# Kernel tuning notes

Hardware: AMD Instinct MI355X
Metric: run time of the kernel (lower is better)

Reference implementation:

```python
import math
import jax, jax.numpy as jnp
import numpy as np
from jax import lax

B, L, C_IN = 8, 1024, 64
D_MODEL, N_HEADS, D_FF, E_LAYERS, FACTOR = 512, 8, 2048, 3, 5


def conv1d_circ(x, w):
    # x [B,L,Cin], w [Cout,Cin,K]; torch Conv1d with padding_mode='circular'
    pad = (w.shape[-1] - 1) // 2
    xp = jnp.pad(x, ((0, 0), (pad, pad), (0, 0)), mode='wrap')
    return lax.conv_general_dilated(xp, jnp.transpose(w, (2, 1, 0)), (1,), 'VALID',
                                    dimension_numbers=('NWC', 'WIO', 'NWC'))


def pos_emb(Lq, d):
    pos = jnp.arange(Lq, dtype=jnp.float32)[:, None]
    div = jnp.exp(jnp.arange(0, d, 2, dtype=jnp.float32) * (-math.log(10000.0) / d))
    pe = jnp.zeros((Lq, d), dtype=jnp.float32)
    pe = pe.at[:, 0::2].set(jnp.sin(pos * div)).at[:, 1::2].set(jnp.cos(pos * div))
    return pe


def layer_norm(x, g, b, eps=1e-5):
    m = x.mean(-1, keepdims=True)
    v = ((x - m) ** 2).mean(-1, keepdims=True)
    return (x - m) / jnp.sqrt(v + eps) * g + b


def prob_attention(Q, K, V, rkey):
    # ProbSparse self-attention (mask_flag=False). Q,K,V: [B,H,L,D]
    Bq, H, Lq, D = Q.shape
    U = min(FACTOR * int(math.ceil(math.log(Lq))), Lq)  # sample_k == n_top since L_Q == L_K
    idx = jax.random.randint(rkey, (Lq, U), 0, Lq)       # per-query sampled key indices
    Ks = jnp.take(K, idx, axis=2)                        # [B,H,L,U,D]
    QKs = jnp.einsum('bhld,bhlud->bhlu', Q, Ks)          # sampled scores
    M = QKs.max(-1) - QKs.sum(-1) / Lq                   # sparsity measure (sum / L_K)
    _, top = lax.top_k(M, U)                             # [B,H,U] top-u query indices
    Qr = jnp.take_along_axis(Q, top[..., None], axis=2)  # [B,H,U,D]
    scores = jnp.einsum('bhud,bhld->bhul', Qr, K) * (1.0 / math.sqrt(D))
    attn = jax.nn.softmax(scores, axis=-1)
    upd = jnp.einsum('bhul,bhld->bhud', attn, V)
    # initial context = mean of V broadcast over queries; scatter updates at top-u
    ctx = jnp.broadcast_to(V.mean(axis=2, keepdims=True), (Bq, H, Lq, D))
    bi = jnp.arange(Bq)[:, None, None]
    hi = jnp.arange(H)[None, :, None]
    ctx = ctx.at[bi, hi, top].set(upd)
    return ctx


def attn_block(x, Wq, bq, Wk, bk, Wv, bv, Wo, bo, rkey):
    Bq, Lq, Dm = x.shape
    Dh = Dm // N_HEADS
    q = (x @ Wq.T + bq).reshape(Bq, Lq, N_HEADS, Dh).transpose(0, 2, 1, 3)
    k = (x @ Wk.T + bk).reshape(Bq, Lq, N_HEADS, Dh).transpose(0, 2, 1, 3)
    v = (x @ Wv.T + bv).reshape(Bq, Lq, N_HEADS, Dh).transpose(0, 2, 1, 3)
    ctx = prob_attention(q, k, v, rkey)
    out = ctx.transpose(0, 2, 1, 3).reshape(Bq, Lq, Dm)
    return out @ Wo.T + bo


def distil_conv(x, w, b, g, be):
    # Conv1d(k=3, circular) -> BatchNorm1d (batch stats) -> ELU -> MaxPool1d(3,2,1)
    y = conv1d_circ(x, w) + b
    mu = y.mean((0, 1))
    var = ((y - mu) ** 2).mean((0, 1))
    y = (y - mu) / jnp.sqrt(var + 1e-5) * g + be
    y = jax.nn.elu(y)
    y = lax.reduce_window(y, -jnp.inf, lax.max, (1, 3, 1), (1, 2, 1),
                          ((0, 0), (1, 1), (0, 0)))
    return y


def forward(x_enc, tok_w, Wq, bq, Wk, bk, Wv, bv, Wo, bo, c1w, c1b, c2w, c2b,
            n1g, n1b, n2g, n2b, dcw, dcb, bng, bnb, fng, fnb):
    x = x_enc + 1e-10
    x = conv1d_circ(x, tok_w) + pos_emb(x.shape[1], D_MODEL)  # embedding (dropout=0)
    for l in range(E_LAYERS):
        rkey = jax.random.fold_in(jax.random.key(42), l)
        x = x + attn_block(x, Wq[l], bq[l], Wk[l], bk[l], Wv[l], bv[l], Wo[l], bo[l], rkey)
        y = x = layer_norm(x, n1g[l], n1b[l])
        y = jax.nn.relu(y @ c1w[l].T + c1b[l])   # Conv1d k=1 == linear
        y = y @ c2w[l].T + c2b[l]
        x = layer_norm(x + y, n2g[l], n2b[l])
        if l < E_LAYERS - 1:
            x = distil_conv(x, dcw[l], dcb[l], bng[l], bnb[l])
    x = layer_norm(x, fng, fnb)
    return x.mean(axis=1)  # [B, D_MODEL]


def setup_inputs() -> dict:
    key = jax.random.key(0)
    ks = jax.random.split(key, 12)
    s = 0.02
    E = E_LAYERS
    return {
        'x_enc': jax.random.normal(ks[0], (B, L, C_IN), jnp.float32),
        'tok_w': jax.random.normal(ks[1], (D_MODEL, C_IN, 3), jnp.float32) * s,
        'Wq': jax.random.normal(ks[2], (E, D_MODEL, D_MODEL), jnp.float32) * s,
        'bq': jnp.zeros((E, D_MODEL), jnp.float32),
        'Wk': jax.random.normal(ks[3], (E, D_MODEL, D_MODEL), jnp.float32) * s,
        'bk': jnp.zeros((E, D_MODEL), jnp.float32),
        'Wv': jax.random.normal(ks[4], (E, D_MODEL, D_MODEL), jnp.float32) * s,
        'bv': jnp.zeros((E, D_MODEL), jnp.float32),
        'Wo': jax.random.normal(ks[5], (E, D_MODEL, D_MODEL), jnp.float32) * s,
        'bo': jnp.zeros((E, D_MODEL), jnp.float32),
        'c1w': jax.random.normal(ks[6], (E, D_FF, D_MODEL), jnp.float32) * s,
        'c1b': jnp.zeros((E, D_FF), jnp.float32),
        'c2w': jax.random.normal(ks[7], (E, D_MODEL, D_FF), jnp.float32) * s,
        'c2b': jnp.zeros((E, D_MODEL), jnp.float32),
        'n1g': jnp.ones((E, D_MODEL), jnp.float32),
        'n1b': jnp.zeros((E, D_MODEL), jnp.float32),
        'n2g': jnp.ones((E, D_MODEL), jnp.float32),
        'n2b': jnp.zeros((E, D_MODEL), jnp.float32),
        'dcw': jax.random.normal(ks[8], (E - 1, D_MODEL, D_MODEL, 3), jnp.float32) * s,
        'dcb': jnp.zeros((E - 1, D_MODEL), jnp.float32),
        'bng': jnp.ones((E - 1, D_MODEL), jnp.float32),
        'bnb': jnp.zeros((E - 1, D_MODEL), jnp.float32),
        'fng': jnp.ones((D_MODEL,), jnp.float32),
        'fnb': jnp.zeros((D_MODEL,), jnp.float32),
    }


def reference(x_enc, tok_w, Wq, bq, Wk, bk, Wv, bv, Wo, bo, c1w, c1b, c2w, c2b,
              n1g, n1b, n2g, n2b, dcw, dcb, bng, bnb, fng, fnb):
    return forward(x_enc, tok_w, Wq, bq, Wk, bk, Wv, bv, Wo, bo, c1w, c1b, c2w, c2b,
                   n1g, n1b, n2g, n2b, dcw, dcb, bng, bnb, fng, fnb)
```

## Files before the change

kernel.cpp:

```cpp
#include <hip/hip_runtime.h>
#include <hip/hip_bf16.h>
#include <math.h>

typedef __hip_bfloat16 bf16;
typedef short bf16x8 __attribute__((ext_vector_type(8)));
typedef float f32x4 __attribute__((ext_vector_type(4)));

__device__ inline short f2bs(float x) {
  bf16 h = __float2bfloat16(x);
  return *reinterpret_cast<short*>(&h);
}

__device__ inline void threefry2x32(unsigned k0, unsigned k1,
                                    unsigned x0, unsigned x1,
                                    unsigned& o0, unsigned& o1) {
  unsigned ks[3] = {k0, k1, k0 ^ k1 ^ 0x1BD11BDAu};
  const int rot[2][4] = {{13, 15, 26, 6}, {17, 29, 16, 24}};
  x0 += ks[0];
  x1 += ks[1];
  #pragma unroll
  for (int i = 0; i < 5; i++) {
    const int* r = rot[i & 1];
    #pragma unroll
    for (int j = 0; j < 4; j++) {
      x0 += x1;
      x1 = (x1 << r[j]) | (x1 >> (32 - r[j]));
      x1 ^= x0;
    }
    x0 += ks[(i + 1) % 3];
    x1 += ks[(i + 2) % 3] + (unsigned)(i + 1);
  }
  o0 = x0;
  o1 = x1;
}

__global__ void idx_kernel(int* __restrict__ idx, int L, int U, int layer) {
  int total = L * U, half = total / 2;
  int i = blockIdx.x * blockDim.x + threadIdx.x;
  if (i >= half) return;
  unsigned k0, k1;
  threefry2x32(0u, 42u, 0u, (unsigned)layer, k0, k1);
  unsigned o0, o1;
  threefry2x32(k0, k1, (unsigned)i, (unsigned)(half + i), o0, o1);
  idx[i] = (int)(o0 & (unsigned)(L - 1));
  idx[half + i] = (int)(o1 & (unsigned)(L - 1));
}

template <int BM, int BN>
__global__ __launch_bounds__(256) void bgemm_t(
    const bf16* __restrict__ A, const bf16* __restrict__ W,
    const float* __restrict__ bias, const float* __restrict__ R, int rmod,
    float* __restrict__ C, bf16* __restrict__ Cb,
    int M, int N, int K, int relu, int outmode) {
  constexpr int MR = BM / 32;
  constexpr int NR = BN / 32;
  __shared__ bf16 As[BM * 32];
  __shared__ bf16 Ws[BN * 32];
  int tid = threadIdx.x;
  int lane = tid & 63, w = tid >> 6;
  size_t row0 = (size_t)blockIdx.x * BM, col0 = (size_t)blockIdx.y * BN;
  int srow = (w << 4) + (lane >> 2);
  int scol = (lane & 3) << 3;
  const bf16* ag0 = A + (row0 + srow) * K + scol;
  const bf16* wg0 = W + (col0 + srow) * K + scol;
  int wb0 = (w << 9) + (lane << 3);
  int wr = (w >> 1) * (BM / 2), wc = (w & 1) * (BN / 2);
  int fr = lane & 15, fk = (lane >> 4) << 3;
  f32x4 acc[MR][NR] = {};
  bf16x8 ra0, ra1, rw0, rw1;
  ra0 = *(const bf16x8*)ag0;
  if constexpr (BM == 128) ra1 = *(const bf16x8*)(ag0 + 64 * K);
  rw0 = *(const bf16x8*)wg0;
  if constexpr (BN == 128) rw1 = *(const bf16x8*)(wg0 + 64 * K);
  for (int k0 = 0; k0 < K; k0 += 32) {
    __syncthreads();
    *(bf16x8*)(As + wb0) = ra0;
    if constexpr (BM == 128) *(bf16x8*)(As + wb0 + 2048) = ra1;
    *(bf16x8*)(Ws + wb0) = rw0;
    if constexpr (BN == 128) *(bf16x8*)(Ws + wb0 + 2048) = rw1;
    if (k0 + 32 < K) {
      ag0 += 32; wg0 += 32;
      ra0 = *(const bf16x8*)ag0;
      if constexpr (BM == 128) ra1 = *(const bf16x8*)(ag0 + 64 * K);
      rw0 = *(const bf16x8*)wg0;
      if constexpr (BN == 128) rw1 = *(const bf16x8*)(wg0 + 64 * K);
    }
    __syncthreads();
    bf16x8 af[MR], bfv[NR];
    #pragma unroll
    for (int m = 0; m < MR; m++)
      af[m] = *(const bf16x8*)(As + (wr + m * 16 + fr) * 32 + fk);
    #pragma unroll
    for (int n = 0; n < NR; n++)
      bfv[n] = *(const bf16x8*)(Ws + (wc + n * 16 + fr) * 32 + fk);
    #pragma unroll
    for (int m = 0; m < MR; m++)
      #pragma unroll
      for (int n = 0; n < NR; n++)
        acc[m][n] = __builtin_amdgcn_mfma_f32_16x16x32_bf16(af[m], bfv[n], acc[m][n], 0, 0, 0);
  }
  int cr = (lane >> 4) << 2;
  int cc0 = lane & 15;
  #pragma unroll
  for (int m = 0; m < MR; m++) {
    #pragma unroll
    for (int n = 0; n < NR; n++) {
      #pragma unroll
      for (int r = 0; r < 4; r++) {
        size_t rr = row0 + wr + m * 16 + cr + r;
        size_t cc = col0 + wc + n * 16 + cc0;
        float v = acc[m][n][r];
        if (bias) v += bias[cc];
        if (R) v += rmod ? R[(rr % rmod) * N + cc] : R[rr * N + cc];
        if (relu) v = fmaxf(v, 0.f);
        if (outmode != 2) C[rr * N + cc] = v;
        if (outmode) Cb[rr * N + cc] = __float2bfloat16(v);
      }
    }
  }
}

__global__ void castw_kernel(const float* __restrict__ wq, const float* __restrict__ wk,
                             const float* __restrict__ wv, const float* __restrict__ wo,
                             const float* __restrict__ c1, const float* __restrict__ c2,
                             bf16* __restrict__ wqkv, bf16* __restrict__ wob,
                             bf16* __restrict__ c1b, bf16* __restrict__ c2b) {
  int i = blockIdx.x * 256 + threadIdx.x;
  if (i >= 786432) return;
  const float* s;
  bf16* d;
  int j;
  if (i < 196608) { s = (i < 65536) ? wq : (i < 131072) ? wk : wv;
                    j = i & 65535; j += (i >> 16) * 65536; s = (i < 65536) ? wq : (i < 131072) ? wk : wv;
                    float4 v = ((const float4*)s)[i & 65535];
                    d = wqkv + (size_t)(i) * 4;
                    d[0] = __float2bfloat16(v.x); d[1] = __float2bfloat16(v.y);
                    d[2] = __float2bfloat16(v.z); d[3] = __float2bfloat16(v.w);
                    return; }
  if (i < 262144) { s = wo; j = i - 196608; d = wob + (size_t)j * 4; }
  else if (i < 524288) { s = c1; j = i - 262144; d = c1b + (size_t)j * 4; }
  else { s = c2; j = i - 524288; d = c2b + (size_t)j * 4; }
  float4 v = ((const float4*)s)[j];
  d[0] = __float2bfloat16(v.x); d[1] = __float2bfloat16(v.y);
  d[2] = __float2bfloat16(v.z); d[3] = __float2bfloat16(v.w);
}

__global__ void catb3_kernel(const float* __restrict__ a, const float* __restrict__ b,
                             const float* __restrict__ c, float* __restrict__ d) {
  int i = blockIdx.x * 256 + threadIdx.x;
  if (i >= 1536) return;
  d[i] = (i < 512) ? a[i] : (i < 1024) ? b[i - 512] : c[i - 1024];
}

__global__ void cast4_kernel(const float* __restrict__ s, bf16* __restrict__ d, int n4) {
  int i = blockIdx.x * 256 + threadIdx.x;
  if (i >= n4) return;
  float4 v = ((const float4*)s)[i];
  d[i * 4 + 0] = __float2bfloat16(v.x);
  d[i * 4 + 1] = __float2bfloat16(v.y);
  d[i * 4 + 2] = __float2bfloat16(v.z);
  d[i * 4 + 3] = __float2bfloat16(v.w);
}

__global__ void wperm_kernel(const float* __restrict__ w, bf16* __restrict__ wcol) {
  int i = blockIdx.x * 256 + threadIdx.x;
  if (i >= 512 * 1536) return;
  int o = i / 1536, r = i % 1536, k = r / 512, c = r % 512;
  wcol[i] = __float2bfloat16(w[o * 1536 + c * 3 + k]);
}

__global__ void tokperm_kernel(const float* __restrict__ w, bf16* __restrict__ d) {
  int i = blockIdx.x * 256 + threadIdx.x;
  if (i >= 512 * 192) return;
  int o = i / 192, r = i % 192, k = r / 64, c = r % 64;
  d[i] = __float2bfloat16(w[o * 192 + c * 3 + k]);
}

__global__ void pe_kernel(float* __restrict__ PE) {
  int t = blockIdx.x, o = threadIdx.x;
  int i2 = o >> 1;
  float div = expf((float)(2 * i2) * (-9.210340371976184f / 512.f));
  float ang = (float)t * div;
  PE[t * 512 + o] = (o & 1) ? cosf(ang) : sinf(ang);
}

__global__ void im2col_e_kernel(const float* __restrict__ x, bf16* __restrict__ d,
                                int B, int L) {
  size_t i = (size_t)blockIdx.x * 256 + threadIdx.x;
  if (i >= (size_t)B * L * 192) return;
  int j = (int)(i % 192);
  size_t row = i / 192;
  int k = j >> 6, c = j & 63;
  int t = (int)(row % L), b = (int)(row / L);
  int ts = (t - 1 + k) & (L - 1);
  d[i] = __float2bfloat16(x[((size_t)(b * L + ts)) * 64 + c] + 1e-10f);
}

__global__ __launch_bounds__(256) void sparsity_kernel(
    const float* __restrict__ QKV, const int* __restrict__ idx,
    float* __restrict__ M, int B, int H, int L, int U) {
  int wid = blockIdx.x * 4 + (threadIdx.x >> 6);
  if (wid >= B * H * L) return;
  int lane = threadIdx.x & 63;
  int t = wid % L, h = (wid / L) % H, b = wid / (L * H);
  int ul = lane >> 4;
  int j = lane & 15;
  const float* qrow = QKV + ((size_t)(b * L + t)) * 1536 + h * 64;
  float4 q4 = *(const float4*)(qrow + j * 4);
  const float* kbase = QKV + (size_t)b * L * 1536 + 512 + h * 64;
  const int* irow = idx + t * U;
  float mx = -INFINITY, sm = 0.f;
  int iters = (U + 3) >> 2;
  for (int i = 0; i < iters; i++) {
    int u = i * 4 + ul;
    bool valid = (u < U);
    int kt = valid ? irow[u] : 0;
    float4 k4 = *(const float4*)(kbase + (size_t)kt * 1536 + j * 4);
    float part = q4.x * k4.x + q4.y * k4.y + q4.z * k4.z + q4.w * k4.w;
    #pragma unroll
    for (int off = 1; off < 16; off <<= 1) part += __shfl_xor(part, off);
    if (valid) { mx = fmaxf(mx, part); sm += part; }
  }
  #pragma unroll
  for (int off = 16; off < 64; off <<= 1) {
    mx = fmaxf(mx, __shfl_xor(mx, off));
    sm += __shfl_xor(sm, off);
  }
  if (lane == 0) M[wid] = mx - sm / (float)L;
}

__global__ __launch_bounds__(1024) void topk_kernel(
    const float* __restrict__ M, int* __restrict__ top, int L, int U) {
  __shared__ float wv[16];
  __shared__ int wi[16];
  __shared__ int best_s;
  int bh = blockIdx.x, tid = threadIdx.x;
  int lane = tid & 63, w = tid >> 6;
  float v = (tid < L) ? M[(size_t)bh * L + tid] : -INFINITY;
  int myt = tid;
  for (int it = 0; it < U; it++) {
    float bv = v;
    int bi = myt;
    #pragma unroll
    for (int off = 32; off; off >>= 1) {
      float ov = __shfl_xor(bv, off);
      int oi = __shfl_xor(bi, off);
      if (ov > bv || (ov == bv && oi < bi)) { bv = ov; bi = oi; }
    }
    if (lane == 0) { wv[w] = bv; wi[w] = bi; }
    __syncthreads();
    if (w == 0) {
      float v2 = (lane < 16) ? wv[lane] : -INFINITY;
      int i2 = (lane < 16) ? wi[lane] : 0x7fffffff;
      #pragma unroll
      for (int off = 8; off; off >>= 1) {
        float ov = __shfl_xor(v2, off);
        int oi = __shfl_xor(i2, off);
        if (ov > v2 || (ov == v2 && oi < i2)) { v2 = ov; i2 = oi; }
      }
      if (lane == 0) { best_s = i2; top[bh * U + it] = i2; }
    }
    __syncthreads();
    if (myt == best_s) v = -INFINITY;
  }
}

__global__ __launch_bounds__(512) void vmean_part_kernel(
    const float* __restrict__ QKV, float* __restrict__ VP, int L, int segs) {
  int b = blockIdx.x, s = blockIdx.y, c = threadIdx.x;
  int per = L / segs;
  const float* vb = QKV + ((size_t)(b * L + s * per)) * 1536 + 1024 + c;
  float acc = 0.f;
  for (int t = 0; t < per; t++) acc += vb[(size_t)t * 1536];
  VP[((size_t)(b * segs + s)) * 512 + c] = acc;
}

__global__ void vmean_reduce_kernel(const float* __restrict__ VP, float* __restrict__ Vmean,
                                    int segs, int L) {
  int i = blockIdx.x * 256 + threadIdx.x;
  if (i >= 8 * 512) return;
  int b = i >> 9, c = i & 511;
  float acc = 0.f;
  for (int s = 0; s < segs; s++) acc += VP[((size_t)(b * segs + s)) * 512 + c];
  Vmean[i] = acc / (float)L;
}

__global__ void bcast_ctx_kernel(const float* __restrict__ Vmean, bf16* __restrict__ ATTb,
                                 int B, int L) {
  size_t i = (size_t)blockIdx.x * 256 + threadIdx.x;
  if (i >= (size_t)B * L * 512) return;
  int c = (int)(i % 512);
  int b = (int)(i / ((size_t)512 * L));
  ATTb[i] = __float2bfloat16(Vmean[b * 512 + c]);
}

__global__ __launch_bounds__(256) void attn_mfma_kernel(
    const float* __restrict__ QKV, const int* __restrict__ top,
    bf16* __restrict__ ATTb, int B, int H, int L, int U) {
  __shared__ short q_lds[64 * 72];
  __shared__ short k_lds[64 * 72];
  __shared__ short vt_lds[64 * 72];
  __shared__ short p_lds[4][16 * 72];
  int bh = blockIdx.x;
  int h = bh & 7, b = bh >> 3;
  int tid = threadIdx.x;
  int lane = tid & 63, w = tid >> 6;
  int r = tid >> 2, q4 = tid & 3, c0 = q4 << 4;
  int fr = lane & 15, fk = (lane >> 4) << 3, g = lane >> 4;

  {
    short tmp[16];
    if (r < U) {
      int tq = top[bh * U + r];
      const float* src = QKV + ((size_t)(b * L + tq)) * 1536 + h * 64 + c0;
      #pragma unroll
      for (int i = 0; i < 4; i++) {
        float4 v = ((const float4*)src)[i];
        tmp[i * 4 + 0] = f2bs(v.x); tmp[i * 4 + 1] = f2bs(v.y);
        tmp[i * 4 + 2] = f2bs(v.z); tmp[i * 4 + 3] = f2bs(v.w);
      }
    } else {
      #pragma unroll
      for (int i = 0; i < 16; i++) tmp[i] = 0;
    }
    *(bf16x8*)&q_lds[r * 72 + c0] = *(bf16x8*)&tmp[0];
    *(bf16x8*)&q_lds[r * 72 + c0 + 8] = *(bf16x8*)&tmp[8];
  }
  __syncthreads();
  bf16x8 aq0 = *(const bf16x8*)&q_lds[(w * 16 + fr) * 72 + fk];
  bf16x8 aq1 = *(const bf16x8*)&q_lds[(w * 16 + fr) * 72 + 32 + fk];

  f32x4 ctx[4] = {};
  float m_run[4], l_run[4];
  #pragma unroll
  for (int i = 0; i < 4; i++) { m_run[i] = -INFINITY; l_run[i] = 0.f; }

  for (int t0 = 0; t0 < L; t0 += 64) {
    __syncthreads();
    {
      const float* ks = QKV + ((size_t)(b * L + t0 + r)) * 1536 + 512 + h * 64 + c0;
      const float* vs = ks + 512;
      short kt[16];
      #pragma unroll
      for (int i = 0; i < 4; i++) {
        float4 v = ((const float4*)ks)[i];
        kt[i * 4 + 0] = f2bs(v.x); kt[i * 4 + 1] = f2bs(v.y);
        kt[i * 4 + 2] = f2bs(v.z); kt[i * 4 + 3] = f2bs(v.w);
      }
      *(bf16x8*)&k_lds[r * 72 + c0] = *(bf16x8*)&kt[0];
      *(bf16x8*)&k_lds[r * 72 + c0 + 8] = *(bf16x8*)&kt[8];
      #pragma unroll
      for (int i = 0; i < 4; i++) {
        float4 v = ((const float4*)vs)[i];
        vt_lds[(c0 + i * 4 + 0) * 72 + r] = f2bs(v.x);
        vt_lds[(c0 + i * 4 + 1) * 72 + r] = f2bs(v.y);
        vt_lds[(c0 + i * 4 + 2) * 72 + r] = f2bs(v.z);
        vt_lds[(c0 + i * 4 + 3) * 72 + r] = f2bs(v.w);
      }
    }
    __syncthreads();
    f32x4 s[4];
    #pragma unroll
    for (int n = 0; n < 4; n++) {
      bf16x8 b0 = *(const bf16x8*)&k_lds[(n * 16 + fr) * 72 + fk];
      bf16x8 b1 = *(const bf16x8*)&k_lds[(n * 16 + fr) * 72 + 32 + fk];
      f32x4 z = {};
      z = __builtin_amdgcn_mfma_f32_16x16x32_bf16(aq0, b0, z, 0, 0, 0);
      s[n] = __builtin_amdgcn_mfma_f32_16x16x32_bf16(aq1, b1, z, 0, 0, 0);
    }
    #pragma unroll
    for (int n = 0; n < 4; n++)
      #pragma unroll
      for (int rg = 0; rg < 4; rg++) s[n][rg] *= 0.125f;
    #pragma unroll
    for (int rg = 0; rg < 4; rg++) {
      float tm = fmaxf(fmaxf(s[0][rg], s[1][rg]), fmaxf(s[2][rg], s[3][rg]));
      #pragma unroll
      for (int off = 1; off < 16; off <<= 1) tm = fmaxf(tm, __shfl_xor(tm, off));
      float mnew = fmaxf(m_run[rg], tm);
      float sc_old = expf(m_run[rg] - mnew);
      float rowsum = 0.f;
      #pragma unroll
      for (int n = 0; n < 4; n++) {
        float p = expf(s[n][rg] - mnew);
        s[n][rg] = p;
        rowsum += p;
      }
      #pragma unroll
      for (int off = 1; off < 16; off <<= 1) rowsum += __shfl_xor(rowsum, off);
      l_run[rg] = l_run[rg] * sc_old + rowsum;
      m_run[rg] = mnew;
      #pragma unroll
      for (int nd = 0; nd < 4; nd++) ctx[nd][rg] *= sc_old;
    }
    short* pw = p_lds[w];
    #pragma unroll
    for (int n = 0; n < 4; n++)
      #pragma unroll
      for (int rg = 0; rg < 4; rg++)
        pw[(g * 4 + rg) * 72 + n * 16 + fr] = f2bs(s[n][rg]);
    bf16x8 pa0 = *(const bf16x8*)&pw[fr * 72 + fk];
    bf16x8 pa1 = *(const bf16x8*)&pw[fr * 72 + 32 + fk];
    #pragma unroll
    for (int nd = 0; nd < 4; nd++) {
      bf16x8 v0 = *(const bf16x8*)&vt_lds[(nd * 16 + fr) * 72 + fk];
      bf16x8 v1 = *(const bf16x8*)&vt_lds[(nd * 16 + fr) * 72 + 32 + fk];
      ctx[nd] = __builtin_amdgcn_mfma_f32_16x16x32_bf16(pa0, v0, ctx[nd], 0, 0, 0);
      ctx[nd] = __builtin_amdgcn_mfma_f32_16x16x32_bf16(pa1, v1, ctx[nd], 0, 0, 0);
    }
  }
  #pragma unroll
  for (int rg = 0; rg < 4; rg++) {
    int qq = w * 16 + g * 4 + rg;
    if (qq < U) {
      int tq = top[bh * U + qq];
      float inv = 1.f / l_run[rg];
      #pragma unroll
      for (int nd = 0; nd < 4; nd++) {
        int d = nd * 16 + fr;
        ATTb[((size_t)(b * L + tq)) * 512 + h * 64 + d] =
            __float2bfloat16(ctx[nd][rg] * inv);
      }
    }
  }
}

__global__ __launch_bounds__(256) void ln_kernel(
    const float* __restrict__ Xin, const float* __restrict__ g,
    const float* __restrict__ bta, float* __restrict__ Xout,
    bf16* __restrict__ Xoutb, int rows) {
  __shared__ float part[8];
  int r = blockIdx.x, tid = threadIdx.x;
  int lane = tid & 63, w = tid >> 6;
  const float* xr = Xin + (size_t)r * 512;
  float v0 = xr[tid], v1 = xr[tid + 256];
  float s = v0 + v1;
  #pragma unroll
  for (int off = 1; off < 64; off <<= 1) s += __shfl_xor(s, off);
  if (lane == 0) part[w] = s;
  __syncthreads();
  float mean = (part[0] + part[1] + part[2] + part[3]) * (1.f / 512.f);
  float d0 = v0 - mean, d1 = v1 - mean;
  float q = d0 * d0 + d1 * d1;
  #pragma unroll
  for (int off = 1; off < 64; off <<= 1) q += __shfl_xor(q, off);
  if (lane == 0) part[4 + w] = q;
  __syncthreads();
  float var = (part[4] + part[5] + part[6] + part[7]) * (1.f / 512.f);
  float rs = rsqrtf(var + 1e-5f);
  float o0 = d0 * rs * g[tid] + bta[tid];
  float o1 = d1 * rs * g[tid + 256] + bta[tid + 256];
  float* out = Xout + (size_t)r * 512;
  out[tid] = o0;
  out[tid + 256] = o1;
  if (Xoutb) {
    Xoutb[(size_t)r * 512 + tid] = __float2bfloat16(o0);
    Xoutb[(size_t)r * 512 + tid + 256] = __float2bfloat16(o1);
  }
}

__global__ void im2col_kernel(const float* __restrict__ X, bf16* __restrict__ XCOL,
                              int B, int L) {
  size_t i = (size_t)blockIdx.x * 256 + threadIdx.x;
  size_t total = (size_t)B * L * 1536;
  if (i >= total) return;
  int c = (int)(i % 512);
  int k = (int)((i / 512) % 3);
  size_t row = i / 1536;
  int t = (int)(row % L), b = (int)(row / L);
  int ts = (t - 1 + k + L) % L;
  XCOL[i] = __float2bfloat16(X[((size_t)(b * L + ts)) * 512 + c]);
}

__global__ void zero_kernel(float* p, int n) {
  int i = blockIdx.x * 256 + threadIdx.x;
  if (i < n) p[i] = 0.f;
}

__global__ __launch_bounds__(256) void bnstat_kernel(
    const float* __restrict__ Y, float* __restrict__ acc, int rows) {
  int tid = threadIdx.x;
  int c0 = tid, c1 = tid + 256;
  float s0 = 0, s1 = 0, q0 = 0, q1 = 0;
  for (int r = blockIdx.x; r < rows; r += gridDim.x) {
    float v0 = Y[(size_t)r * 512 + c0];
    float v1 = Y[(size_t)r * 512 + c1];
    s0 += v0; q0 += v0 * v0;
    s1 += v1; q1 += v1 * v1;
  }
  atomicAdd(&acc[c0], s0);
  atomicAdd(&acc[c1], s1);
  atomicAdd(&acc[512 + c0], q0);
  atomicAdd(&acc[512 + c1], q1);
}

__global__ void bnpool_kernel(const float* __restrict__ Y, const float* __restrict__ acc,
                              const float* __restrict__ g, const float* __restrict__ be,
                              float* __restrict__ Xout, bf16* __restrict__ Xoutb,
                              int B, int L, int rows) {
  int Lout = L / 2;
  size_t i = (size_t)blockIdx.x * 256 + threadIdx.x;
  if (i >= (size_t)B * Lout * 512) return;
  int c = (int)(i % 512);
  size_t orow = i / 512;
  int to = (int)(orow % Lout), b = (int)(orow / Lout);
  float mu = acc[c] / (float)rows;
  float var = acc[512 + c] / (float)rows - mu * mu;
  float rs = rsqrtf(var + 1e-5f) * g[c];
  float mx = -INFINITY;
  #pragma unroll
  for (int dj = -1; dj <= 1; dj++) {
    int j = 2 * to + dj;
    if (j < 0 || j >= L) continue;
    float v = (Y[((size_t)(b * L + j)) * 512 + c] - mu) * rs + be[c];
    v = v > 0.f ? v : expm1f(v);
    mx = fmaxf(mx, v);
  }
  Xout[i] = mx;
  Xoutb[i] = __float2bfloat16(mx);
}

__global__ void meanrows_part_kernel(const float* __restrict__ Xin, float* __restrict__ MP,
                                     int L, int segs) {
  int b = blockIdx.x, s = blockIdx.y, d = threadIdx.x;
  int per = L / segs;
  const float* base = Xin + ((size_t)(b * L + s * per)) * 512 + d;
  float acc = 0.f;
  for (int t = 0; t < per; t++) acc += base[(size_t)t * 512];
  MP[((size_t)(b * segs + s)) * 512 + d] = acc;
}

__global__ void meanrows_red_kernel(const float* __restrict__ MP, float* __restrict__ out,
                                    int segs, int L) {
  int i = blockIdx.x * 256 + threadIdx.x;
  if (i >= 8 * 512) return;
  int b = i >> 9, c = i & 511;
  float acc = 0.f;
  for (int s = 0; s < segs; s++) acc += MP[((size_t)(b * segs + s)) * 512 + c];
  out[i] = acc / (float)L;
}

extern "C" void kernel_launch(void* const* d_in, const int* in_sizes, int n_in,
                              void* d_out, int out_size, void* d_ws, size_t ws_size,
                              hipStream_t stream) {
  const float* x_enc = (const float*)d_in[0];
  const float* tok_w = (const float*)d_in[1];
  const float* Wq = (const float*)d_in[2];
  const float* bq = (const float*)d_in[3];
  const float* Wk = (const float*)d_in[4];
  const float* bk = (const float*)d_in[5];
  const float* Wv = (const float*)d_in[6];
  const float* bv = (const float*)d_in[7];
  const float* Wo = (const float*)d_in[8];
  const float* bo = (const float*)d_in[9];
  const float* c1w = (const float*)d_in[10];
  const float* c1b = (const float*)d_in[11];
  const float* c2w = (const float*)d_in[12];
  const float* c2b = (const float*)d_in[13];
  const float* n1g = (const float*)d_in[14];
  const float* n1b = (const float*)d_in[15];
  const float* n2g = (const float*)d_in[16];
  const float* n2b = (const float*)d_in[17];
  const float* dcw = (const float*)d_in[18];
  const float* dcb = (const float*)d_in[19];
  const float* bng = (const float*)d_in[20];
  const float* bnb = (const float*)d_in[21];
  const float* fng = (const float*)d_in[22];
  const float* fnb = (const float*)d_in[23];

  const int B = 8, H = 8;
  const size_t NX = 4194304;

  float* ws = (float*)d_ws;
  float* X    = ws;
  float* XLN  = ws + NX;
  float* QKVf = ws + 2 * NX;
  bf16* H2b   = (bf16*)(ws + 2 * NX);
  float* Yc   = ws + 2 * NX;
  bf16* XCOLb = (bf16*)(ws + 4 * NX);
  bf16* INb   = (bf16*)(ws + 5 * NX);
  bf16* ATTb  = (bf16*)(ws + 5 * NX + NX / 2);
  float* WB   = ws + 6 * NX;
  bf16* WQKVb = (bf16*)(WB);
  bf16* Wob  = (bf16*)(WB + 393216);
  bf16* c1wb = (bf16*)(WB + 524288);
  bf16* c2wb = (bf16*)(WB + 1048576);
  bf16* wcvb = (bf16*)(WB + 1572864);
  bf16* tokwb = (bf16*)(WB + 1966080);
  float* PE   = WB + 2015232;
  float* MBUF = PE + 524288;
  float* VMEAN = MBUF + 65536;
  float* BNACC = VMEAN + 4096;
  int* IDX = (int*)(BNACC + 1024);
  int* TOP = IDX + 35840;
  float* VPART = (float*)(TOP + 2240);
  float* BQKV = VPART + 131072;

  pe_kernel<<<1024, 512, 0, stream>>>(PE);
  tokperm_kernel<<<(512 * 192 + 255) / 256, 256, 0, stream>>>(tok_w, tokwb);
  im2col_e_kernel<<<(int)(((size_t)B * 1024 * 192 + 255) / 256), 256, 0, stream>>>(
      x_enc, INb, B, 1024);
  bgemm_t<64, 64><<<dim3(128, 8), 256, 0, stream>>>(INb, tokwb, nullptr, PE, 1024,
                                                    X, nullptr, 8192, 512, 192, 0, 0);
  cast4_kernel<<<4096, 256, 0, stream>>>(X, INb, 1048576);

  int L = 1024;
  for (int l = 0; l < 3; l++) {
    int U = (L == 256) ? 30 : 35;
    int rows = B * L;
    dim3 g64(rows / 64, 8);

    castw_kernel<<<3072, 256, 0, stream>>>(
        Wq + (size_t)l * 262144, Wk + (size_t)l * 262144, Wv + (size_t)l * 262144,
        Wo + (size_t)l * 262144, c1w + (size_t)l * 1048576, c2w + (size_t)l * 1048576,
        WQKVb, Wob, c1wb, c2wb);
    catb3_kernel<<<6, 256, 0, stream>>>(bq + l * 512, bk + l * 512, bv + l * 512, BQKV);
    if (l < 2)
      wperm_kernel<<<3072, 256, 0, stream>>>(dcw + (size_t)l * 786432, wcvb);

    bgemm_t<64, 64><<<dim3(rows / 64, 24), 256, 0, stream>>>(
        INb, WQKVb, BQKV, nullptr, 0, QKVf, nullptr, rows, 1536, 512, 0, 0);

    int half = L * U / 2;
    idx_kernel<<<(half + 255) / 256, 256, 0, stream>>>(IDX, L, U, l);
    sparsity_kernel<<<(B * H * L + 3) / 4, 256, 0, stream>>>(QKVf, IDX, MBUF, B, H, L, U);
    topk_kernel<<<B * H, 1024, 0, stream>>>(MBUF, TOP, L, U);
    vmean_part_kernel<<<dim3(B, 32), 512, 0, stream>>>(QKVf, VPART, L, 32);
    vmean_reduce_kernel<<<16, 256, 0, stream>>>(VPART, VMEAN, 32, L);
    bcast_ctx_kernel<<<(rows * 512) / 256, 256, 0, stream>>>(VMEAN, ATTb, B, L);
    attn_mfma_kernel<<<B * H, 256, 0, stream>>>(QKVf, TOP, ATTb, B, H, L, U);

    bgemm_t<64, 64><<<g64, 256, 0, stream>>>(ATTb, Wob, bo + l * 512, X, 0,
                                             X, nullptr, rows, 512, 512, 0, 0);
    ln_kernel<<<rows, 256, 0, stream>>>(X, n1g + l * 512, n1b + l * 512, XLN, INb, rows);
    bgemm_t<64, 64><<<dim3(rows / 64, 32), 256, 0, stream>>>(
        INb, c1wb, c1b + l * 2048, nullptr, 0, nullptr, H2b, rows, 2048, 512, 1, 2);
    bgemm_t<64, 64><<<g64, 256, 0, stream>>>(H2b, c2wb, c2b + l * 512, XLN, 0,
                                             X, nullptr, rows, 512, 2048, 0, 0);
    ln_kernel<<<rows, 256, 0, stream>>>(X, n2g + l * 512, n2b + l * 512, X, nullptr, rows);

    if (l < 2) {
      im2col_kernel<<<(int)(((size_t)rows * 1536) / 256), 256, 0, stream>>>(X, XCOLb, B, L);
      bgemm_t<64, 64><<<g64, 256, 0, stream>>>(XCOLb, wcvb, dcb + l * 512, nullptr, 0,
                                               Yc, nullptr, rows, 512, 1536, 0, 0);
      zero_kernel<<<4, 256, 0, stream>>>(BNACC, 1024);
      bnstat_kernel<<<128, 256, 0, stream>>>(Yc, BNACC, rows);
      bnpool_kernel<<<(rows / 2 * 512) / 256, 256, 0, stream>>>(
          Yc, BNACC, bng + l * 512, bnb + l * 512, X, INb, B, L, rows);
      L >>= 1;
    }
  }

  int rowsF = B * L;
  ln_kernel<<<rowsF, 256, 0, stream>>>(X, fng, fnb, XLN, nullptr, rowsF);
  meanrows_part_kernel<<<dim3(8, 8), 512, 0, stream>>>(XLN, VPART, L, 8);
  meanrows_red_kernel<<<16, 256, 0, stream>>>(VPART, (float*)d_out, 8, L);
}
```

Baseline: 947.1 us.

## Switch GEMMs to 2-wave 64x64 tiles, fuse embed cast, remap sparsity blocks

Replaces the 4-wave 64x64 GEMM with a 2-wave variant in which each wave computes a 32x64 sub-tile with more MFMAs per LDS fragment load, giving more work per thread and fewer threads per block. The token-embedding GEMM now writes its bf16 copy directly, which removes the separate cast kernel. The sparsity kernel uses 8 lanes per sampled key and an XCD-aware block-to-(b,h) mapping so that blocks sharing the same K rows tend to land on the same die. Fewer waves per block can lower latency hiding unless occupancy rises to make up for it.

```diff
diff --git a/kernel.cpp b/kernel.cpp
--- a/kernel.cpp
+++ b/kernel.cpp
@@ -46,69 +46,65 @@
   idx[half + i] = (int)(o1 & (unsigned)(L - 1));
 }
 
-template <int BM, int BN>
-__global__ __launch_bounds__(256) void bgemm_t(
+__global__ __launch_bounds__(128) void bgemm2(
     const bf16* __restrict__ A, const bf16* __restrict__ W,
     const float* __restrict__ bias, const float* __restrict__ R, int rmod,
     float* __restrict__ C, bf16* __restrict__ Cb,
     int M, int N, int K, int relu, int outmode) {
-  constexpr int MR = BM / 32;
-  constexpr int NR = BN / 32;
-  __shared__ bf16 As[BM * 32];
-  __shared__ bf16 Ws[BN * 32];
+  __shared__ bf16 As[64 * 32];
+  __shared__ bf16 Ws[64 * 32];
   int tid = threadIdx.x;
   int lane = tid & 63, w = tid >> 6;
-  size_t row0 = (size_t)blockIdx.x * BM, col0 = (size_t)blockIdx.y * BN;
-  int srow = (w << 4) + (lane >> 2);
-  int scol = (lane & 3) << 3;
-  const bf16* ag0 = A + (row0 + srow) * K + scol;
-  const bf16* wg0 = W + (col0 + srow) * K + scol;
-  int wb0 = (w << 9) + (lane << 3);
-  int wr = (w >> 1) * (BM / 2), wc = (w & 1) * (BN / 2);
+  size_t row0 = (size_t)blockIdx.x * 64, col0 = (size_t)blockIdx.y * 64;
+  int srow = tid >> 1;
+  int scol = (tid & 1) << 4;
+  const bf16* ag = A + (row0 + srow) * K + scol;
+  const bf16* wg = W + (col0 + srow) * K + scol;
+  int wb = (srow << 5) + scol;
   int fr = lane & 15, fk = (lane >> 4) << 3;
-  f32x4 acc[MR][NR] = {};
-  bf16x8 ra0, ra1, rw0, rw1;
-  ra0 = *(const bf16x8*)ag0;
-  if constexpr (BM == 128) ra1 = *(const bf16x8*)(ag0 + 64 * K);
-  rw0 = *(const bf16x8*)wg0;
-  if constexpr (BN == 128) rw1 = *(const bf16x8*)(wg0 + 64 * K);
+  int wr = w << 5;
+  f32x4 acc[2][4] = {};
+  bf16x8 ra0 = *(const bf16x8*)ag;
+  bf16x8 ra1 = *(const bf16x8*)(ag + 8);
+  bf16x8 rw0 = *(const bf16x8*)wg;
+  bf16x8 rw1 = *(const bf16x8*)(wg + 8);
   for (int k0 = 0; k0 < K; k0 += 32) {
     __syncthreads();
-    *(bf16x8*)(As + wb0) = ra0;
-    if constexpr (BM == 128) *(bf16x8*)(As + wb0 + 2048) = ra1;
-    *(bf16x8*)(Ws + wb0) = rw0;
-    if constexpr (BN == 128) *(bf16x8*)(Ws + wb0 + 2048) = rw1;
+    *(bf16x8*)(As + wb) = ra0;
+    *(bf16x8*)(As + wb + 8) = ra1;
+    *(bf16x8*)(Ws + wb) = rw0;
+    *(bf16x8*)(Ws + wb + 8) = rw1;
     if (k0 + 32 < K) {
-      ag0 += 32; wg0 += 32;
-      ra0 = *(const bf16x8*)ag0;
-      if constexpr (BM == 128) ra1 = *(const bf16x8*)(ag0 + 64 * K);
-      rw0 = *(const bf16x8*)wg0;
-      if constexpr (BN == 128) rw1 = *(const bf16x8*)(wg0 + 64 * K);
+      ag += 32; wg += 32;
+      ra0 = *(const bf16x8*)ag;
+      ra1 = *(const bf16x8*)(ag + 8);
+      rw0 = *(const bf16x8*)wg;
+      rw1 = *(const bf16x8*)(wg + 8);
     }
     __syncthreads();
-    bf16x8 af[MR], bfv[NR];
-    #pragma unroll
-    for (int m = 0; m < MR; m++)
+    bf16x8 af[2], bfv[4];
+    #pragma unroll
+    for (int m = 0; m < 2; m++)
       af[m] = *(const bf16x8*)(As + (wr + m * 16 + fr) * 32 + fk);
     #pragma unroll
-    for (int n = 0; n < NR; n++)
-      bfv[n] = *(const bf16x8*)(Ws + (wc + n * 16 + fr) * 32 + fk);
-    #pragma unroll
-    for (int m = 0; m < MR; m++)
-      #pragma unroll
-      for (int n = 0; n < NR; n++)
+    for (int n = 0; n < 4; n++)
+      bfv[n] = *(const bf16x8*)(Ws + (n * 16 + fr) * 32 + fk);
+    #pragma unroll
+    for (int m = 0; m < 2; m++)
+      #pragma unroll
+      for (int n = 0; n < 4; n++)
         acc[m][n] = __builtin_amdgcn_mfma_f32_16x16x32_bf16(af[m], bfv[n], acc[m][n], 0, 0, 0);
   }
   int cr = (lane >> 4) << 2;
   int cc0 = lane & 15;
   #pragma unroll
-  for (int m = 0; m < MR; m++) {
-    #pragma unroll
-    for (int n = 0; n < NR; n++) {
+  for (int m = 0; m < 2; m++) {
+    #pragma unroll
+    for (int n = 0; n < 4; n++) {
       #pragma unroll
       for (int r = 0; r < 4; r++) {
         size_t rr = row0 + wr + m * 16 + cr + r;
-        size_t cc = col0 + wc + n * 16 + cc0;
+        size_t cc = col0 + n * 16 + cc0;
         float v = acc[m][n][r];
         if (bias) v += bias[cc];
         if (R) v += rmod ? R[(rr % rmod) * N + cc] : R[rr * N + cc];
@@ -130,13 +126,14 @@
   const float* s;
   bf16* d;
   int j;
-  if (i < 196608) { s = (i < 65536) ? wq : (i < 131072) ? wk : wv;
-                    j = i & 65535; j += (i >> 16) * 65536; s = (i < 65536) ? wq : (i < 131072) ? wk : wv;
-                    float4 v = ((const float4*)s)[i & 65535];
-                    d = wqkv + (size_t)(i) * 4;
-                    d[0] = __float2bfloat16(v.x); d[1] = __float2bfloat16(v.y);
-                    d[2] = __float2bfloat16(v.z); d[3] = __float2bfloat16(v.w);
-                    return; }
+  if (i < 196608) {
+    s = (i < 65536) ? wq : (i < 131072) ? wk : wv;
+    float4 v = ((const float4*)s)[i & 65535];
+    d = wqkv + (size_t)i * 4;
+    d[0] = __float2bfloat16(v.x); d[1] = __float2bfloat16(v.y);
+    d[2] = __float2bfloat16(v.z); d[3] = __float2bfloat16(v.w);
+    return;
+  }
   if (i < 262144) { s = wo; j = i - 196608; d = wob + (size_t)j * 4; }
   else if (i < 524288) { s = c1; j = i - 262144; d = c1b + (size_t)j * 4; }
   else { s = c2; j = i - 524288; d = c2b + (size_t)j * 4; }
@@ -150,16 +147,6 @@
   int i = blockIdx.x * 256 + threadIdx.x;
   if (i >= 1536) return;
   d[i] = (i < 512) ? a[i] : (i < 1024) ? b[i - 512] : c[i - 1024];
-}
-
-__global__ void cast4_kernel(const float* __restrict__ s, bf16* __restrict__ d, int n4) {
-  int i = blockIdx.x * 256 + threadIdx.x;
-  if (i >= n4) return;
-  float4 v = ((const float4*)s)[i];
-  d[i * 4 + 0] = __float2bfloat16(v.x);
-  d[i * 4 + 1] = __float2bfloat16(v.y);
-  d[i * 4 + 2] = __float2bfloat16(v.z);
-  d[i * 4 + 3] = __float2bfloat16(v.w);
 }
 
 __global__ void wperm_kernel(const float* __restrict__ w, bf16* __restrict__ wcol) {
@@ -199,34 +186,42 @@
 __global__ __launch_bounds__(256) void sparsity_kernel(
     const float* __restrict__ QKV, const int* __restrict__ idx,
     float* __restrict__ M, int B, int H, int L, int U) {
-  int wid = blockIdx.x * 4 + (threadIdx.x >> 6);
-  if (wid >= B * H * L) return;
+  int tpb = L >> 2;
+  int xcd = blockIdx.x & 7, slot = blockIdx.x >> 3;
+  int bh = xcd + ((slot / tpb) << 3);
+  int tb = slot % tpb;
+  int wave = threadIdx.x >> 6;
+  int t = tb * 4 + wave;
   int lane = threadIdx.x & 63;
-  int t = wid % L, h = (wid / L) % H, b = wid / (L * H);
-  int ul = lane >> 4;
-  int j = lane & 15;
-  const float* qrow = QKV + ((size_t)(b * L + t)) * 1536 + h * 64;
-  float4 q4 = *(const float4*)(qrow + j * 4);
-  const float* kbase = QKV + (size_t)b * L * 1536 + 512 + h * 64;
+  int h = bh & 7, b = bh >> 3;
+  int ul = lane >> 3;
+  int j = lane & 7;
+  const float* qrow = QKV + ((size_t)(b * L + t)) * 1536 + h * 64 + j * 8;
+  float4 qa = *(const float4*)qrow;
+  float4 qb = *(const float4*)(qrow + 4);
+  const float* kbase = QKV + (size_t)b * L * 1536 + 512 + h * 64 + j * 8;
   const int* irow = idx + t * U;
   float mx = -INFINITY, sm = 0.f;
-  int iters = (U + 3) >> 2;
+  int iters = (U + 7) >> 3;
   for (int i = 0; i < iters; i++) {
-    int u = i * 4 + ul;
+    int u = i * 8 + ul;
     bool valid = (u < U);
     int kt = valid ? irow[u] : 0;
-    float4 k4 = *(const float4*)(kbase + (size_t)kt * 1536 + j * 4);
-    float part = q4.x * k4.x + q4.y * k4.y + q4.z * k4.z + q4.w * k4.w;
-    #pragma unroll
-    for (int off = 1; off < 16; off <<= 1) part += __shfl_xor(part, off);
+    const float* kr = kbase + (size_t)kt * 1536;
+    float4 ka = *(const float4*)kr;
+    float4 kb = *(const float4*)(kr + 4);
+    float part = qa.x * ka.x + qa.y * ka.y + qa.z * ka.z + qa.w * ka.w +
+                 qb.x * kb.x + qb.y * kb.y + qb.z * kb.z + qb.w * kb.w;
+    #pragma unroll
+    for (int off = 1; off < 8; off <<= 1) part += __shfl_xor(part, off);
     if (valid) { mx = fmaxf(mx, part); sm += part; }
   }
   #pragma unroll
-  for (int off = 16; off < 64; off <<= 1) {
+  for (int off = 8; off < 64; off <<= 1) {
     mx = fmaxf(mx, __shfl_xor(mx, off));
     sm += __shfl_xor(sm, off);
   }
-  if (lane == 0) M[wid] = mx - sm / (float)L;
+  if (lane == 0) M[(size_t)bh * L + t] = mx - sm / (float)L;
 }
 
 __global__ __launch_bounds__(1024) void topk_kernel(
@@ -600,9 +595,8 @@
   tokperm_kernel<<<(512 * 192 + 255) / 256, 256, 0, stream>>>(tok_w, tokwb);
   im2col_e_kernel<<<(int)(((size_t)B * 1024 * 192 + 255) / 256), 256, 0, stream>>>(
       x_enc, INb, B, 1024);
-  bgemm_t<64, 64><<<dim3(128, 8), 256, 0, stream>>>(INb, tokwb, nullptr, PE, 1024,
-                                                    X, nullptr, 8192, 512, 192, 0, 0);
-  cast4_kernel<<<4096, 256, 0, stream>>>(X, INb, 1048576);
+  bgemm2<<<dim3(128, 8), 128, 0, stream>>>(INb, tokwb, nullptr, PE, 1024,
+                                           X, INb, 8192, 512, 192, 0, 1);
 
   int L = 1024;
   for (int l = 0; l < 3; l++) {
@@ -618,31 +612,31 @@
     if (l < 2)
       wperm_kernel<<<3072, 256, 0, stream>>>(dcw + (size_t)l * 786432, wcvb);
 
-    bgemm_t<64, 64><<<dim3(rows / 64, 24), 256, 0, stream>>>(
+    bgemm2<<<dim3(rows / 64, 24), 128, 0, stream>>>(
         INb, WQKVb, BQKV, nullptr, 0, QKVf, nullptr, rows, 1536, 512, 0, 0);
 
     int half = L * U / 2;
     idx_kernel<<<(half + 255) / 256, 256, 0, stream>>>(IDX, L, U, l);
-    sparsity_kernel<<<(B * H * L + 3) / 4, 256, 0, stream>>>(QKVf, IDX, MBUF, B, H, L, U);
+    sparsity_kernel<<<(B * H * L) / 4, 256, 0, stream>>>(QKVf, IDX, MBUF, B, H, L, U);
     topk_kernel<<<B * H, 1024, 0, stream>>>(MBUF, TOP, L, U);
     vmean_part_kernel<<<dim3(B, 32), 512, 0, stream>>>(QKVf, VPART, L, 32);
     vmean_reduce_kernel<<<16, 256, 0, stream>>>(VPART, VMEAN, 32, L);
     bcast_ctx_kernel<<<(rows * 512) / 256, 256, 0, stream>>>(VMEAN, ATTb, B, L);
     attn_mfma_kernel<<<B * H, 256, 0, stream>>>(QKVf, TOP, ATTb, B, H, L, U);
 
-    bgemm_t<64, 64><<<g64, 256, 0, stream>>>(ATTb, Wob, bo + l * 512, X, 0,
-                                             X, nullptr, rows, 512, 512, 0, 0);
+    bgemm2<<<g64, 128, 0, stream>>>(ATTb, Wob, bo + l * 512, X, 0,
+                                    X, nullptr, rows, 512, 512, 0, 0);
     ln_kernel<<<rows, 256, 0, stream>>>(X, n1g + l * 512, n1b + l * 512, XLN, INb, rows);
-    bgemm_t<64, 64><<<dim3(rows / 64, 32), 256, 0, stream>>>(
+    bgemm2<<<dim3(rows / 64, 32), 128, 0, stream>>>(
         INb, c1wb, c1b + l * 2048, nullptr, 0, nullptr, H2b, rows, 2048, 512, 1, 2);
-    bgemm_t<64, 64><<<g64, 256, 0, stream>>>(H2b, c2wb, c2b + l * 512, XLN, 0,
-                                             X, nullptr, rows, 512, 2048, 0, 0);
+    bgemm2<<<g64, 128, 0, stream>>>(H2b, c2wb, c2b + l * 512, XLN, 0,
+                                    X, nullptr, rows, 512, 2048, 0, 0);
     ln_kernel<<<rows, 256, 0, stream>>>(X, n2g + l * 512, n2b + l * 512, X, nullptr, rows);
 
     if (l < 2) {
       im2col_kernel<<<(int)(((size_t)rows * 1536) / 256), 256, 0, stream>>>(X, XCOLb, B, L);
-      bgemm_t<64, 64><<<g64, 256, 0, stream>>>(XCOLb, wcvb, dcb + l * 512, nullptr, 0,
-                                               Yc, nullptr, rows, 512, 1536, 0, 0);
+      bgemm2<<<g64, 128, 0, stream>>>(XCOLb, wcvb, dcb + l * 512, nullptr, 0,
+                                      Yc, nullptr, rows, 512, 1536, 0, 0);
       zero_kernel<<<4, 256, 0, stream>>>(BNACC, 1024);
       bnstat_kernel<<<128, 256, 0, stream>>>(Yc, BNACC, rows);
       bnpool_kernel<<<(rows / 2 * 512) / 256, 256, 0, stream>>>(
```

Measured after the change: 981.7 us. +3.7%, slower.
